# Optimization experiments

Measured on AMD Instinct MI355X. Metric: run time of the kernel, lower is better.

The kernel has to match this reference:

```python
import math
import jax
import jax.numpy as jnp
import numpy as np

B, N, NPOINT, K = 8, 2048, 512, 16
CIN = 64
MLP = [64, 128, 256]
M_W = 8    # PAConv weight-bank size
HID = 16   # scorenet hidden width
GEOM = 10  # 3 rel-xyz + 1 dist + 3 norm + 3 angles


def setup_inputs():
    key = jax.random.key(0)
    ks = jax.random.split(key, 40)
    inp = {}
    inp['xyz'] = jax.random.normal(ks[0], (B, 3, N), jnp.float32)
    inp['norm'] = jax.random.normal(ks[1], (B, 3, N), jnp.float32)
    inp['X_axis'] = jax.random.normal(ks[2], (B, 3, N), jnp.float32)
    inp['Y_axis'] = jax.random.normal(ks[3], (B, 3, N), jnp.float32)
    inp['points'] = jax.random.normal(ks[4], (B, CIN, N), jnp.float32) * 0.5
    cin = CIN
    ki = 5
    for l, cout in enumerate(MLP):
        inp['w1_%d' % l] = jax.random.normal(ks[ki], (HID, GEOM), jnp.float32) / np.sqrt(GEOM); ki += 1
        inp['b1_%d' % l] = jnp.zeros((HID,), jnp.float32)
        inp['w2_%d' % l] = jax.random.normal(ks[ki], (M_W, HID), jnp.float32) / np.sqrt(HID); ki += 1
        inp['b2_%d' % l] = jnp.zeros((M_W,), jnp.float32)
        inp['bank_%d' % l] = jax.random.normal(ks[ki], (M_W, cin, cout), jnp.float32) / np.sqrt(cin); ki += 1
        if l < len(MLP) - 1:
            inp['gamma_%d' % l] = jnp.ones((cout,), jnp.float32)
            inp['beta_%d' % l] = jnp.zeros((cout,), jnp.float32)
        cin = cout
    return inp


def _group(t, idx):
    # t: (B, C, N), idx: (B, ...) int -> (B, C, ...)
    return jax.vmap(lambda p, i: p[:, i])(t, idx)


def _fps(xyz_t, npoint):
    # xyz_t: (B, N, 3) -> (B, npoint) int32; standard iterative FPS starting at index 0
    b, n, _ = xyz_t.shape
    def body(i, c):
        idxs, dists, far = c
        idxs = idxs.at[:, i].set(far)
        centroid = jnp.take_along_axis(xyz_t, far[:, None, None], axis=1)  # (B,1,3)
        d = jnp.sum((xyz_t - centroid) ** 2, axis=-1)
        dists = jnp.minimum(dists, d)
        return idxs, dists, jnp.argmax(dists, axis=-1).astype(jnp.int32)
    idxs = jnp.zeros((b, npoint), jnp.int32)
    dists = jnp.full((b, n), 1e10, xyz_t.dtype)
    far = jnp.zeros((b,), jnp.int32)
    idxs, _, _ = jax.lax.fori_loop(0, npoint, body, (idxs, dists, far))
    return idxs


def _sqdist(a, b):
    # a: (B, P, 3), b: (B, N, 3) -> (B, P, N)
    return (jnp.sum(a ** 2, -1)[:, :, None] + jnp.sum(b ** 2, -1)[:, None, :]
            - 2.0 * jnp.einsum('bpc,bnc->bpn', a, b))


def _angles(gxyz, gn, gX, gY):
    # all (B, 3, P, K) -> (B, 3, P, K); normalized angles to z(norm)/x/y frame axes
    nn = jnp.linalg.norm(gxyz, axis=1)
    def ang(v):
        c = jnp.sum(gxyz * v, axis=1) / (nn * jnp.linalg.norm(v, axis=1) + 1e-8)
        return jnp.arccos(jnp.clip(c, -1.0, 1.0)) / math.pi
    return jnp.stack([ang(gn), ang(gX), ang(gY)], axis=1)


def _paconv(geom, feats, w1, b1, w2, b2, bank, gamma=None, beta=None, act=True):
    # ScoreNet over geometric channels -> softmax scores over M weight matrices
    h = jax.nn.relu(jnp.einsum('hg,bgpk->bhpk', w1, geom) + b1[None, :, None, None])
    s = jax.nn.softmax(jnp.einsum('mh,bhpk->bmpk', w2, h) + b2[None, :, None, None], axis=1)
    out = jnp.einsum('bcpk,mco,bmpk->bopk', feats, bank, s)
    if gamma is not None:
        mu = out.mean(axis=(0, 2, 3), keepdims=True)
        var = out.var(axis=(0, 2, 3), keepdims=True)
        out = (out - mu) / jnp.sqrt(var + 1e-5) * gamma[None, :, None, None] + beta[None, :, None, None]
    return jax.nn.relu(out) if act else out


def reference(xyz, norm, X_axis, Y_axis, points,
              w1_0, b1_0, w2_0, b2_0, bank_0, gamma_0, beta_0,
              w1_1, b1_1, w2_1, b2_1, bank_1, gamma_1, beta_1,
              w1_2, b1_2, w2_2, b2_2, bank_2):
    xyz_t = jnp.transpose(xyz, (0, 2, 1))           # (B,N,3)
    fidx = _fps(xyz_t, NPOINT)                      # (B,NPOINT)
    new_xyz = _group(xyz, fidx)                     # (B,3,NPOINT)
    sq = _sqdist(jnp.transpose(new_xyz, (0, 2, 1)), xyz_t)  # (B,NPOINT,N)
    idx = jax.lax.top_k(-sq, K)[1]                  # (B,NPOINT,K) ascending distance
    grouped_xyz = _group(xyz, idx) - new_xyz[:, :, :, None]  # (B,3,NPOINT,K)
    dist = jnp.sqrt(jnp.sum(grouped_xyz ** 2, axis=1) + 1e-10)  # (B,NPOINT,K)
    dmin = dist.min(axis=2, keepdims=True)
    dist = (dist - dmin) / (dist.max(axis=2, keepdims=True) - dmin + 1e-10)
    new_points = _group(points, idx)                # (B,CIN,NPOINT,K)
    grouped_norm = _group(norm, idx)
    grouped_X = _group(X_axis, idx)
    grouped_Y = _group(Y_axis, idx)
    grouped_angles = _angles(grouped_xyz, grouped_norm, grouped_X, grouped_Y)
    new_norm = grouped_norm[:, :, :, 0]
    new_X = grouped_X[:, :, :, 0]
    new_Y = grouped_Y[:, :, :, 0]
    geom = jnp.concatenate([grouped_xyz, dist[:, None], grouped_norm, grouped_angles], axis=1)  # (B,10,NPOINT,K)
    new_points = _paconv(geom, new_points, w1_0, b1_0, w2_0, b2_0, bank_0, gamma_0, beta_0, act=True)
    new_points = _paconv(geom, new_points, w1_1, b1_1, w2_1, b2_1, bank_1, gamma_1, beta_1, act=True)
    new_points = _paconv(geom, new_points, w1_2, b1_2, w2_2, b2_2, bank_2, None, None, act=False)
    new_points = jnp.max(new_points, axis=3)        # (B,MLP[-1],NPOINT)
    return (new_xyz, new_norm, new_X, new_Y, new_points)
```

## Files before the change

### kernel.cpp

```cpp
#include <hip/hip_runtime.h>
#include <math.h>

#define NBATCH 8
#define NPTS   2048
#define NPOINT 512
#define KNB    16
#define NROWS  (NBATCH*NPOINT*KNB)

#define TRANS_BASE  NBATCH
#define ZERO_BID    (NBATCH + 256)
#define CONV_BASE   (NBATCH + 257)
#define KNN_BASE    (NBATCH + 257 + 704)
#define MEGA_GRID   (KNN_BASE + 1024)
#define RCTR_TARGET 960

typedef unsigned short ushort_t;
typedef unsigned int   uint_t;
typedef unsigned long long ull_t;
typedef __attribute__((ext_vector_type(8))) short  short8;
typedef __attribute__((ext_vector_type(4))) float  f32x4;
typedef __attribute__((ext_vector_type(2))) float  f32x2;

#define B0_OFF 0
#define B1_OFF 32768
#define B2_OFF 98304
#define BT_TOT 360448

#define LDS_BARRIER() asm volatile("s_waitcnt lgkmcnt(0)\n\ts_barrier" ::: "memory")

__device__ __align__(16) int      g_fidx [NBATCH * NPOINT];
__device__ __align__(16) int      g_fready[NBATCH * NPOINT];
__device__            int      g_rctr = 0;
__device__ __align__(16) int      g_knn [NROWS];
__device__ __align__(16) float    g_sums[1024];
__device__ __align__(16) float    g_pT  [NBATCH * NPTS * 64];
__device__ __align__(16) float    g_S   [(size_t)3 * NROWS * 8];
__device__ __align__(16) float    g_act1[(size_t)NROWS * 64];
__device__ __align__(16) float    g_act2[(size_t)NROWS * 128];
__device__ __align__(16) ushort_t g_bankF[BT_TOT];

__device__ __forceinline__ ushort_t f2bf(float f) {
    uint_t u = __float_as_uint(f);
    return (ushort_t)((u + 0x7FFFu + ((u >> 16) & 1u)) >> 16);
}

template<int CTRL>
__device__ __forceinline__ ull_t dpp_u64(ull_t k) {
    int lo = (int)(uint_t)k;
    int hi = (int)(uint_t)(k >> 32);
    int slo = __builtin_amdgcn_update_dpp(0, lo, CTRL, 0xF, 0xF, true);
    int shi = __builtin_amdgcn_update_dpp(0, hi, CTRL, 0xF, 0xF, true);
    return ((ull_t)(uint_t)shi << 32) | (uint_t)slo;
}

__device__ __forceinline__ ull_t dpp_max_u64(ull_t key) {
    { ull_t s = dpp_u64<0x111>(key); if (s > key) key = s; }
    { ull_t s = dpp_u64<0x112>(key); if (s > key) key = s; }
    { ull_t s = dpp_u64<0x114>(key); if (s > key) key = s; }
    { ull_t s = dpp_u64<0x118>(key); if (s > key) key = s; }
    { ull_t s = dpp_u64<0x142>(key); if (s > key) key = s; }
    { ull_t s = dpp_u64<0x143>(key); if (s > key) key = s; }
    return key;
}

template<int CTRL>
__device__ __forceinline__ uint_t dpp_u32(uint_t v) {
    return (uint_t)__builtin_amdgcn_update_dpp(0, (int)v, CTRL, 0xF, 0xF, true);
}

__device__ __forceinline__ uint_t dpp_max_u32(uint_t v) {
    { uint_t s = dpp_u32<0x111>(v); if (s > v) v = s; }
    { uint_t s = dpp_u32<0x112>(v); if (s > v) v = s; }
    { uint_t s = dpp_u32<0x114>(v); if (s > v) v = s; }
    { uint_t s = dpp_u32<0x118>(v); if (s > v) v = s; }
    { uint_t s = dpp_u32<0x142>(v); if (s > v) v = s; }
    { uint_t s = dpp_u32<0x143>(v); if (s > v) v = s; }
    return v;
}

template<int COUT>
__device__ __forceinline__ void bank_frag2(const float* __restrict__ bank,
                                           uint_t* __restrict__ dst, int le) {
    const int j = le & 7;
    const int lane = (le >> 3) & 63;
    const int rem = le >> 9;
    constexpr int NTL = COUT / 16;
    const int nt = rem % NTL;
    const int kc = rem / NTL;
    const int q = lane >> 4, nlo = lane & 15;
    const int k = kc * 32 + q * 8 + j;
    const int n = nt * 16 + nlo;
    const float f0 = bank[(size_t)k * COUT + n];
    const float f1 = bank[(size_t)(k + 1) * COUT + n];
    dst[le >> 1] = (uint_t)f2bf(f0) | ((uint_t)f2bf(f1) << 16);
}

__global__ __launch_bounds__(256, 5) void mega_kernel(
    const float* __restrict__ xyz, const float* __restrict__ points,
    const float* __restrict__ bank0, const float* __restrict__ bank1,
    const float* __restrict__ bank2, float* __restrict__ dout,
    const float* __restrict__ nrm, const float* __restrict__ Xa,
    const float* __restrict__ Ya,
    const float* __restrict__ w1_0, const float* __restrict__ b1_0,
    const float* __restrict__ w2_0, const float* __restrict__ b2_0,
    const float* __restrict__ w1_1, const float* __restrict__ b1_1,
    const float* __restrict__ w2_1, const float* __restrict__ b2_1,
    const float* __restrict__ w1_2, const float* __restrict__ b1_2,
    const float* __restrict__ w2_2, const float* __restrict__ b2_2) {
    __shared__ float smem[3 * NPTS];
    __shared__ ull_t s_key[2][4];
    const int bid = blockIdx.x;
    const int t = threadIdx.x;

    if (bid >= NBATCH) {
        if (bid < ZERO_BID) {
            float (*tile)[65] = reinterpret_cast<float(*)[65]>(smem);
            const int blk = bid - TRANS_BASE;
            const int b = blk >> 5;
            const int n0 = (blk & 31) * 64;
            const int lane = t & 63, q = t >> 6;
            #pragma unroll
            for (int i = 0; i < 16; ++i) {
                int c = q * 16 + i;
                tile[c][lane] = points[(b * 64 + c) * NPTS + n0 + lane];
            }
            __syncthreads();
            #pragma unroll
            for (int i = 0; i < 16; ++i) {
                int n = q * 16 + i;
                g_pT[(size_t)(b * NPTS + n0 + n) * 64 + lane] = tile[lane][n];
            }
            __syncthreads();
            if (t == 0)
                __hip_atomic_fetch_add(&g_rctr, 1, __ATOMIC_RELEASE,
                                       __HIP_MEMORY_SCOPE_AGENT);
            return;
        } else if (bid == ZERO_BID) {
            g_sums[256 + t] = 0.0f;
            return;
        } else if (bid < KNN_BASE) {
            const int le = ((bid - CONV_BASE) * 256 + t) << 1;
            if (le < 32768) {
                bank_frag2<64>(bank0, reinterpret_cast<uint_t*>(g_bankF + B0_OFF), le);
            } else if (le < 98304) {
                bank_frag2<128>(bank1, reinterpret_cast<uint_t*>(g_bankF + B1_OFF), le - 32768);
            } else {
                bank_frag2<256>(bank2, reinterpret_cast<uint_t*>(g_bankF + B2_OFF), le - 98304);
            }
            __syncthreads();
            if (t == 0)
                __hip_atomic_fetch_add(&g_rctr, 1, __ATOMIC_RELEASE,
                                       __HIP_MEMORY_SCOPE_AGENT);
            return;
        }

        {
            const float* w1p[3] = {w1_0, w1_1, w1_2};
            const float* b1p[3] = {b1_0, b1_1, b1_2};
            const float* w2p[3] = {w2_0, w2_1, w2_2};
            const float* b2p[3] = {b2_0, b2_1, b2_2};
            #pragma unroll
            for (int l = 0; l < 3; ++l) {
                if (t < 160) smem[l * 160 + t] = w1p[l][t];
                if (t < 16)  smem[480 + l * 16 + t] = b1p[l][t];
                if (t < 128) smem[528 + l * 128 + t] = w2p[l][t];
                if (t < 8)   smem[912 + l * 8 + t] = b2p[l][t];
            }
        }
        __syncthreads();

        const int wave = (bid - KNN_BASE) * 4 + (t >> 6);
        const int lane = t & 63;
        const int b = wave >> 9;
        const int p = wave & 511;
        const float* xb = xyz + b * 3 * NPTS;

        int fv = __hip_atomic_load(&g_fready[wave], __ATOMIC_RELAXED,
                                   __HIP_MEMORY_SCOPE_AGENT);
        while (fv == 0) {
            __builtin_amdgcn_s_sleep(15);
            fv = __hip_atomic_load(&g_fready[wave], __ATOMIC_RELAXED,
                                   __HIP_MEMORY_SCOPE_AGENT);
        }
        if (lane == 0)
            __hip_atomic_store(&g_fready[wave], 0, __ATOMIC_RELAXED,
                               __HIP_MEMORY_SCOPE_AGENT);
        const int fi = (fv - 1) & (NPTS - 1);
        int nmine = 0;

        {
            #pragma clang fp contract(off)
            float ax = xb[fi];
            float ay = xb[NPTS + fi];
            float az = xb[2*NPTS + fi];
            float sa = ax*ax + ay*ay; sa = sa + az*az;
            float d[32];
            #pragma unroll
            for (int j = 0; j < 32; ++j) {
                int pp = j * 64 + lane;
                float bx = xb[pp];
                float by = xb[NPTS + pp];
                float bz = xb[2*NPTS + pp];
                float sb = bx*bx + by*by; sb = sb + bz*bz;
                float dot = ax*bx + ay*by; dot = dot + az*bz;
                float t1 = sa + sb;
                float t2 = 2.0f * dot;
                d[j] = t1 - t2;
            }
            for (int r = 0; r < KNB; ++r) {
                float best = 1e30f; int bi = 0x7fffffff;
                #pragma unroll
                for (int j = 0; j < 32; ++j) {
                    if (d[j] < best) { best = d[j]; bi = j * 64 + lane; }
                }
                uint_t ub = __float_as_uint(best);
                ub = (ub & 0x80000000u) ? ~ub : (ub | 0x80000000u);
                ull_t key = ((ull_t)(~ub) << 32) | (uint_t)(~bi);
                key = dpp_max_u64(key);
                uint_t wlo = (uint_t)__builtin_amdgcn_readlane((int)(uint_t)key, 63);
                bi = (int)(~wlo) & (NPTS - 1);
                if (lane == 0) g_knn[wave * KNB + r] = bi;
                if (lane == r) nmine = bi;
                int rl = bi & 63, rs = bi >> 6;
                if (lane == rl) {
                    #pragma unroll
                    for (int j = 0; j < 32; ++j) if (j == rs) d[j] = 1e30f;
                }
            }
        }

        {
            const int n0 = __builtin_amdgcn_readlane(nmine, 0) & (NPTS - 1);
            if (lane < 12) {
                const int arr = lane / 3, a = lane % 3;
                const float* src = (arr == 0) ? xyz : (arr == 1) ? nrm
                                 : (arr == 2) ? Xa : Ya;
                const int idx = (arr == 0) ? fi : n0;
                dout[arr * 12288 + (b*3 + a) * NPOINT + p] =
                    src[(b*3 + a) * NPTS + idx];
            }
        }

        if (lane < 16) {
            const int row = wave * KNB + lane;
            const int n = nmine & (NPTS - 1);
            const float* nb = nrm + b * 3 * NPTS;
            const float* Xb = Xa  + b * 3 * NPTS;
            const float* Yb = Ya  + b * 3 * NPTS;
            float gx, gy, gz, sq, draw, nnv;
            {
                #pragma clang fp contract(off)
                gx = xb[n]        - xb[fi];
                gy = xb[NPTS + n] - xb[NPTS + fi];
                gz = xb[2*NPTS+n] - xb[2*NPTS+fi];
                sq = gx*gx + gy*gy;
                sq = sq + gz*gz;
                draw = sqrtf(sq + 1e-10f);
                nnv = sqrtf(sq);
            }
            float dmin = draw, dmax = draw;
            #pragma unroll
            for (int m = 1; m < 16; m <<= 1) {
                dmin = fminf(dmin, __shfl_xor(dmin, m, 16));
                dmax = fmaxf(dmax, __shfl_xor(dmax, m, 16));
            }
            float dist;
            {
                #pragma clang fp contract(off)
                dist = (draw - dmin) / ((dmax - dmin) + 1e-10f);
            }
            float nx = nb[n], ny = nb[NPTS+n], nz = nb[2*NPTS+n];
            float Xx = Xb[n], Xy = Xb[NPTS+n], Xz = Xb[2*NPTS+n];
            float Yx = Yb[n], Yy = Yb[NPTS+n], Yz = Yb[2*NPTS+n];
            float g[10];
            g[0]=gx; g[1]=gy; g[2]=gz; g[3]=dist; g[4]=nx; g[5]=ny; g[6]=nz;
            {
                float vs[3][3] = {{nx,ny,nz},{Xx,Xy,Xz},{Yx,Yy,Yz}};
                #pragma unroll
                for (int a = 0; a < 3; ++a) {
                    float vx=vs[a][0], vy=vs[a][1], vz=vs[a][2];
                    float dot, nv;
                    {
                        #pragma clang fp contract(off)
                        dot = gx*vx + gy*vy; dot = dot + gz*vz;
                        float s2 = vx*vx + vy*vy; s2 = s2 + vz*vz;
                        nv = sqrtf(s2);
                    }
                    float cc = dot / (nnv * nv + 1e-8f);
                    cc = fminf(1.0f, fmaxf(-1.0f, cc));
                    g[7+a] = acosf(cc) / 3.14159274101257324f;
                }
            }
            #pragma unroll
            for (int l = 0; l < 3; ++l) {
                float h[16];
                #pragma unroll
                for (int i = 0; i < 16; ++i) {
                    float a = smem[480 + l * 16 + i];
                    #pragma unroll
                    for (int j = 0; j < 10; ++j) a += smem[l * 160 + i * 10 + j] * g[j];
                    h[i] = fmaxf(a, 0.0f);
                }
                float e[8]; float mx = -1e30f;
                #pragma unroll
                for (int m = 0; m < 8; ++m) {
                    float a = smem[912 + l * 8 + m];
                    #pragma unroll
                    for (int j = 0; j < 16; ++j) a += smem[528 + l * 128 + m * 16 + j] * h[j];
                    e[m] = a; mx = fmaxf(mx, a);
                }
                float sum = 0.0f;
                #pragma unroll
                for (int m = 0; m < 8; ++m) { e[m] = expf(e[m] - mx); sum += e[m]; }
                #pragma unroll
                for (int m = 0; m < 8; ++m)
                    g_S[(size_t)l * NROWS * 8 + (size_t)row * 8 + m] = e[m] / sum;
            }
        }

        __syncthreads();
        if (t == 0) {
            while (__hip_atomic_load(&g_rctr, __ATOMIC_ACQUIRE,
                                     __HIP_MEMORY_SCOPE_AGENT) < RCTR_TARGET)
                __builtin_amdgcn_s_sleep(8);
        }
        __syncthreads();

        {
            constexpr int NTT0 = 4;
            constexpr int CCM0 = 2;
            ushort_t (*AsP)[64][36] = reinterpret_cast<ushort_t(*)[64][36]>(smem + 1024);
            float* s_rs  = smem + 3328;
            float* s_rss = smem + 3392;
            const int w = t >> 6;
            const int q = lane >> 4, nlo = lane & 15;
            const int row0 = (bid - KNN_BASE) * 64;
            const int arow_i = t >> 2, acg = t & 3;
            const int rr = row0 + arow_i;
            const int rb = rr >> 13;
            const int rn = g_knn[rr] & (NPTS - 1);
            const size_t arow = (size_t)(rb * NPTS + rn) * 64;
            const float* Sb = g_S + (size_t)rr * 8;
            float svv[8];
            #pragma unroll
            for (int m = 0; m < 8; ++m) svv[m] = Sb[m];
            f32x4 acc[4];
            #pragma unroll
            for (int mi = 0; mi < 4; ++mi) acc[mi] = (f32x4){0.f, 0.f, 0.f, 0.f};
            const ushort_t* fbase = g_bankF + B0_OFF + lane * 8;
            union FragU { uint4 u4; uint2 u2[2]; short8 s; };
            FragU B[2];
            B[0].u4 = *reinterpret_cast<const uint4*>(fbase + (size_t)w * 512);
            float vraw[8], vnext[8];
            {
                const float* ap = g_pT + arow + acg * 8;
                float4 fa = *reinterpret_cast<const float4*>(ap);
                float4 fb = *reinterpret_cast<const float4*>(ap + 4);
                vraw[0]=fa.x; vraw[1]=fa.y; vraw[2]=fa.z; vraw[3]=fa.w;
                vraw[4]=fb.x; vraw[5]=fb.y; vraw[6]=fb.z; vraw[7]=fb.w;
            }
            int par = 0;
            for (int cc = 0; cc < CCM0; ++cc) {
                #pragma unroll
                for (int m = 0; m < 8; ++m) {
                    {
                        const float sv = svv[m];
                        uint_t* dst = reinterpret_cast<uint_t*>(&AsP[par][arow_i][acg * 8]);
                        #pragma unroll
                        for (int j = 0; j < 8; j += 2)
                            dst[j >> 1] = (uint_t)f2bf(sv * vraw[j]) |
                                          ((uint_t)f2bf(sv * vraw[j + 1]) << 16);
                    }
                    if (m == 0) {
                        const int ccn = (cc + 1 < CCM0) ? cc + 1 : cc;
                        const float* ap = g_pT + arow + ccn * 32 + acg * 8;
                        float4 fa = *reinterpret_cast<const float4*>(ap);
                        float4 fb = *reinterpret_cast<const float4*>(ap + 4);
                        vnext[0]=fa.x; vnext[1]=fa.y; vnext[2]=fa.z; vnext[3]=fa.w;
                        vnext[4]=fb.x; vnext[5]=fb.y; vnext[6]=fb.z; vnext[7]=fb.w;
                    }
                    {
                        const int kcn = (m < 7) ? ((m + 1) * CCM0 + cc)
                                                : ((cc + 1 < CCM0) ? (cc + 1) : 0);
                        B[(m + 1) & 1].u4 = *reinterpret_cast<const uint4*>(
                            fbase + (size_t)(kcn * NTT0 + w) * 512);
                    }
                    LDS_BARRIER();
                    FragU af[4];
                    #pragma unroll
                    for (int mi = 0; mi < 4; ++mi) {
                        af[mi].u2[0] = *reinterpret_cast<const uint2*>(&AsP[par][mi*16 + nlo][q*8]);
                        af[mi].u2[1] = *reinterpret_cast<const uint2*>(&AsP[par][mi*16 + nlo][q*8 + 4]);
                    }
                    #pragma unroll
                    for (int mi = 0; mi < 4; ++mi)
                        acc[mi] = __builtin_amdgcn_mfma_f32_16x16x32_bf16(
                            af[mi].s, B[m & 1].s, acc[mi], 0, 0, 0);
                    par ^= 1;
                }
                #pragma unroll
                for (int j = 0; j < 8; ++j) vraw[j] = vnext[j];
            }
            #pragma unroll
            for (int mi = 0; mi < 4; ++mi)
                #pragma unroll
                for (int r2 = 0; r2 < 4; ++r2)
                    g_act1[(size_t)(row0 + mi*16 + q*4 + r2) * 64 + w*16 + nlo] = acc[mi][r2];
            float s = 0.f, ss = 0.f;
            #pragma unroll
            for (int mi = 0; mi < 4; ++mi) {
                #pragma unroll
                for (int r2 = 0; r2 < 4; ++r2) {
                    float x = acc[mi][r2];
                    s += x; ss += x * x;
                }
            }
            s  += __shfl_xor(s, 16);  s  += __shfl_xor(s, 32);
            ss += __shfl_xor(ss, 16); ss += __shfl_xor(ss, 32);
            if (q == 0) {
                const int c = w * 16 + nlo;
                s_rs[c] = s;
                s_rss[c] = ss;
            }
            __syncthreads();
            if (t < 64) {
                atomicAdd(&g_sums[t], s_rs[t]);
                atomicAdd(&g_sums[64 + t], s_rss[t]);
            }
        }
        return;
    }

    {
        #pragma clang fp contract(off)
        const int b = bid;
        const int lane = t & 63, w = t >> 6;
        const float* xb = xyz + b * 3 * NPTS;
        float* s_x = smem;
        float* s_y = smem + NPTS;
        float* s_z = smem + 2 * NPTS;
        f32x2 xp[4], yp[4], zp[4];
        float d[8];
        {
            const float4* xq = reinterpret_cast<const float4*>(xb + t * 8);
            const float4* yq = reinterpret_cast<const float4*>(xb + NPTS + t * 8);
            const float4* zq = reinterpret_cast<const float4*>(xb + 2 * NPTS + t * 8);
            float4 a0 = xq[0], a1 = xq[1];
            float4 b0 = yq[0], b1 = yq[1];
            float4 c0 = zq[0], c1 = zq[1];
            xp[0] = (f32x2){a0.x, a0.y}; xp[1] = (f32x2){a0.z, a0.w};
            xp[2] = (f32x2){a1.x, a1.y}; xp[3] = (f32x2){a1.z, a1.w};
            yp[0] = (f32x2){b0.x, b0.y}; yp[1] = (f32x2){b0.z, b0.w};
            yp[2] = (f32x2){b1.x, b1.y}; yp[3] = (f32x2){b1.z, b1.w};
            zp[0] = (f32x2){c0.x, c0.y}; zp[1] = (f32x2){c0.z, c0.w};
            zp[2] = (f32x2){c1.x, c1.y}; zp[3] = (f32x2){c1.z, c1.w};
            *reinterpret_cast<float4*>(s_x + t * 8)     = a0;
            *reinterpret_cast<float4*>(s_x + t * 8 + 4) = a1;
            *reinterpret_cast<float4*>(s_y + t * 8)     = b0;
            *reinterpret_cast<float4*>(s_y + t * 8 + 4) = b1;
            *reinterpret_cast<float4*>(s_z + t * 8)     = c0;
            *reinterpret_cast<float4*>(s_z + t * 8 + 4) = c1;
            #pragma unroll
            for (int j = 0; j < 8; ++j) d[j] = 1e10f;
        }
        __syncthreads();
        __builtin_amdgcn_s_setprio(2);
        int far = 0;
        for (int i = 0; i < NPOINT; ++i) {
            if (t == 0) {
                g_fidx[b * NPOINT + i] = far;
                __hip_atomic_store(&g_fready[b * NPOINT + i], far + 1,
                                   __ATOMIC_RELAXED, __HIP_MEMORY_SCOPE_AGENT);
            }
            const float cx = s_x[far], cy = s_y[far], cz = s_z[far];
            const f32x2 cxp = (f32x2){cx, cx};
            const f32x2 cyp = (f32x2){cy, cy};
            const f32x2 czp = (f32x2){cz, cz};
            uint_t bb = 0u;
            #pragma unroll
            for (int a = 0; a < 4; ++a) {
                f32x2 dx = xp[a] - cxp;
                f32x2 dy = yp[a] - cyp;
                f32x2 dz = zp[a] - czp;
                f32x2 s2 = dx*dx + dy*dy;
                s2 = s2 + dz*dz;
                float dn0 = fminf(d[2*a],   s2[0]);
                float dn1 = fminf(d[2*a+1], s2[1]);
                d[2*a] = dn0; d[2*a+1] = dn1;
                uint_t u0 = __float_as_uint(dn0);
                uint_t u1 = __float_as_uint(dn1);
                bb = (u0 > bb) ? u0 : bb;
                bb = (u1 > bb) ? u1 : bb;
            }
            uint_t wm = dpp_max_u32(bb);
            const uint_t wbits = (uint_t)__builtin_amdgcn_readlane((int)wm, 63);
            int li = 8;
            #pragma unroll
            for (int j = 7; j >= 0; --j)
                li = (__float_as_uint(d[j]) == wbits) ? j : li;
            ull_t mk = __ballot(li < 8);
            const int fl = __ffsll((unsigned long long)mk) - 1;
            const int wj = __builtin_amdgcn_readlane(li, fl);
            const int wp = (((w << 6) + fl) << 3) + wj;
            if (lane == 0) s_key[i & 1][w] = ((ull_t)wbits << 32) | (uint_t)(~wp);
            LDS_BARRIER();
            const ull_t* kb = s_key[i & 1];
            ull_t k0 = kb[0], k1 = kb[1], k2 = kb[2], k3 = kb[3];
            if (k1 > k0) k0 = k1;
            if (k3 > k2) k2 = k3;
            if (k2 > k0) k0 = k2;
            far = (int)(~(uint_t)k0) & (NPTS - 1);
        }
    }
}

template<int LAYER, int CIN, int COUT>
__global__ __launch_bounds__(256) void gemm_kernel(const float* __restrict__ gamma,
                                                   const float* __restrict__ beta,
                                                   float* __restrict__ dout) {
    const float* __restrict__ A = (LAYER == 1) ? g_act1 : g_act2;
    float* __restrict__ O = (LAYER == 1) ? g_act2 : dout;
    constexpr int NTT = COUT / 16;
    constexpr int NTW = NTT / 4;
    constexpr int CCM = CIN / 32;
    constexpr int BOFF = (LAYER == 1) ? B1_OFF : B2_OFF;
    __shared__ ushort_t As[2][64][36];
    __shared__ float s_scale[CIN];
    __shared__ float s_shift[CIN];
    __shared__ float s_rs[(LAYER < 2) ? COUT : 1];
    __shared__ float s_rss[(LAYER < 2) ? COUT : 1];

    const int t = threadIdx.x;
    const int lane = t & 63, w = t >> 6;
    const int q = lane >> 4, nlo = lane & 15;
    const int row0 = blockIdx.x * 64;
    const int arow_i = t >> 2, acg = t & 3;

    if constexpr (LAYER == 2) {
        if (blockIdx.x == 0 && t < 128) g_sums[t] = 0.0f;
    }

    {
        const float* sb = (LAYER == 1) ? g_sums : (g_sums + 256);
        if (t < CIN) {
            float mu  = sb[t] * (1.0f / 65536.0f);
            float var = sb[CIN + t] * (1.0f / 65536.0f) - mu * mu;
            var = fmaxf(var, 0.0f);
            float sc = gamma[t] / sqrtf(var + 1e-5f);
            s_scale[t] = sc;
            s_shift[t] = beta[t] - mu * sc;
        }
        __syncthreads();
    }

    const size_t arow = (size_t)(row0 + arow_i) * CIN;
    const float* Sbase = g_S + (size_t)LAYER * NROWS * 8 + (size_t)(row0 + arow_i) * 8;

    float svv[8];
    #pragma unroll
    for (int m = 0; m < 8; ++m) svv[m] = Sbase[m];

    f32x4 acc[4][NTW];
    #pragma unroll
    for (int mi = 0; mi < 4; ++mi)
        #pragma unroll
        for (int ni = 0; ni < NTW; ++ni) acc[mi][ni] = (f32x4){0.f, 0.f, 0.f, 0.f};

    const ushort_t* fbase = g_bankF + BOFF + lane * 8;

    union FragU { uint4 u4; uint2 u2[2]; short8 s; };
    FragU B[2][NTW];
    #pragma unroll
    for (int ni = 0; ni < NTW; ++ni)
        B[0][ni].u4 = *reinterpret_cast<const uint4*>(fbase + (size_t)(w * NTW + ni) * 512);

    float vraw[8], vnext[8];
    {
        const float* ap = A + arow + acg * 8;
        float4 fa = *reinterpret_cast<const float4*>(ap);
        float4 fb = *reinterpret_cast<const float4*>(ap + 4);
        vraw[0]=fa.x; vraw[1]=fa.y; vraw[2]=fa.z; vraw[3]=fa.w;
        vraw[4]=fb.x; vraw[5]=fb.y; vraw[6]=fb.z; vraw[7]=fb.w;
    }

    int par = 0;
    for (int cc = 0; cc < CCM; ++cc) {
        float v[8];
        #pragma unroll
        for (int j = 0; j < 8; ++j) {
            const int c = cc * 32 + acg * 8 + j;
            v[j] = fmaxf(vraw[j] * s_scale[c] + s_shift[c], 0.f);
        }
        #pragma unroll
        for (int m = 0; m < 8; ++m) {
            {
                const float sv = svv[m];
                uint_t* dst = reinterpret_cast<uint_t*>(&As[par][arow_i][acg * 8]);
                #pragma unroll
                for (int j = 0; j < 8; j += 2)
                    dst[j >> 1] = (uint_t)f2bf(sv * v[j]) | ((uint_t)f2bf(sv * v[j+1]) << 16);
            }
            if (m == 0) {
                const int ccn = (cc + 1 < CCM) ? cc + 1 : cc;
                const float* ap = A + arow + ccn * 32 + acg * 8;
                float4 fa = *reinterpret_cast<const float4*>(ap);
                float4 fb = *reinterpret_cast<const float4*>(ap + 4);
                vnext[0]=fa.x; vnext[1]=fa.y; vnext[2]=fa.z; vnext[3]=fa.w;
                vnext[4]=fb.x; vnext[5]=fb.y; vnext[6]=fb.z; vnext[7]=fb.w;
            }
            {
                const int kcn = (m < 7) ? ((m + 1) * CCM + cc)
                                        : ((cc + 1 < CCM) ? (cc + 1) : 0);
                #pragma unroll
                for (int ni = 0; ni < NTW; ++ni)
                    B[(m + 1) & 1][ni].u4 = *reinterpret_cast<const uint4*>(
                        fbase + (size_t)(kcn * NTT + w * NTW + ni) * 512);
            }
            LDS_BARRIER();
            FragU af[4];
            #pragma unroll
            for (int mi = 0; mi < 4; ++mi) {
                af[mi].u2[0] = *reinterpret_cast<const uint2*>(&As[par][mi*16 + nlo][q*8]);
                af[mi].u2[1] = *reinterpret_cast<const uint2*>(&As[par][mi*16 + nlo][q*8 + 4]);
            }
            #pragma unroll
            for (int ni = 0; ni < NTW; ++ni)
                #pragma unroll
                for (int mi = 0; mi < 4; ++mi)
                    acc[mi][ni] = __builtin_amdgcn_mfma_f32_16x16x32_bf16(
                        af[mi].s, B[m & 1][ni].s, acc[mi][ni], 0, 0, 0);
            par ^= 1;
        }
        #pragma unroll
        for (int j = 0; j < 8; ++j) vraw[j] = vnext[j];
    }

    if constexpr (LAYER == 2) {
        const int bp0 = row0 >> 4;
        #pragma unroll
        for (int mi = 0; mi < 4; ++mi) {
            const int bp = bp0 + mi;
            const int b = bp >> 9, p = bp & 511;
            #pragma unroll
            for (int ni = 0; ni < NTW; ++ni) {
                float mv = fmaxf(fmaxf(acc[mi][ni][0], acc[mi][ni][1]),
                                 fmaxf(acc[mi][ni][2], acc[mi][ni][3]));
                mv = fmaxf(mv, __shfl_xor(mv, 16));
                mv = fmaxf(mv, __shfl_xor(mv, 32));
                if (lane < 16) {
                    const int col = w * 64 + ni * 16 + nlo;
                    O[(size_t)(b * 256 + col) * NPOINT + p] = mv;
                }
            }
        }
    } else {
        #pragma unroll
        for (int mi = 0; mi < 4; ++mi)
            #pragma unroll
            for (int ni = 0; ni < NTW; ++ni)
                #pragma unroll
                for (int r2 = 0; r2 < 4; ++r2)
                    O[(size_t)(row0 + mi*16 + q*4 + r2) * COUT + w*NTW*16 + ni*16 + nlo] = acc[mi][ni][r2];
        #pragma unroll
        for (int ni = 0; ni < NTW; ++ni) {
            float s = 0.f, ss = 0.f;
            #pragma unroll
            for (int mi = 0; mi < 4; ++mi) {
                #pragma unroll
                for (int r2 = 0; r2 < 4; ++r2) {
                    float x = acc[mi][ni][r2];
                    s += x; ss += x * x;
                }
            }
            s  += __shfl_xor(s, 16);  s  += __shfl_xor(s, 32);
            ss += __shfl_xor(ss, 16); ss += __shfl_xor(ss, 32);
            if (q == 0) {
                const int c = w * NTW * 16 + ni * 16 + nlo;
                s_rs[c] = s;
                s_rss[c] = ss;
            }
        }
        __syncthreads();
        if (t < COUT) {
            float* sb = g_sums + 256;
            atomicAdd(&sb[t], s_rs[t]);
            atomicAdd(&sb[COUT + t], s_rss[t]);
        }
    }
}

extern "C" void kernel_launch(void* const* d_in, const int* in_sizes, int n_in,
                              void* d_out, int out_size, void* d_ws, size_t ws_size,
                              hipStream_t stream) {
    const float* xyz    = (const float*)d_in[0];
    const float* nrm    = (const float*)d_in[1];
    const float* Xa     = (const float*)d_in[2];
    const float* Ya     = (const float*)d_in[3];
    const float* points = (const float*)d_in[4];
    const float* w1_0 = (const float*)d_in[5];  const float* b1_0 = (const float*)d_in[6];
    const float* w2_0 = (const float*)d_in[7];  const float* b2_0 = (const float*)d_in[8];
    const float* bank0 = (const float*)d_in[9];
    const float* g0 = (const float*)d_in[10];   const float* be0 = (const float*)d_in[11];
    const float* w1_1 = (const float*)d_in[12]; const float* b1_1 = (const float*)d_in[13];
    const float* w2_1 = (const float*)d_in[14]; const float* b2_1 = (const float*)d_in[15];
    const float* bank1 = (const float*)d_in[16];
    const float* g1 = (const float*)d_in[17];   const float* be1 = (const float*)d_in[18];
    const float* w1_2 = (const float*)d_in[19]; const float* b1_2 = (const float*)d_in[20];
    const float* w2_2 = (const float*)d_in[21]; const float* b2_2 = (const float*)d_in[22];
    const float* bank2 = (const float*)d_in[23];
    float* out = (float*)d_out;
    (void)d_ws; (void)ws_size; (void)in_sizes; (void)n_in; (void)out_size;

    mega_kernel<<<MEGA_GRID, 256, 0, stream>>>(xyz, points, bank0, bank1, bank2, out,
                                               nrm, Xa, Ya,
                                               w1_0, b1_0, w2_0, b2_0,
                                               w1_1, b1_1, w2_1, b2_1,
                                               w1_2, b1_2, w2_2, b2_2);
    gemm_kernel<1, 64, 128><<<1024, 256, 0, stream>>>(g0, be0, nullptr);
    gemm_kernel<2, 128, 256><<<1024, 256, 0, stream>>>(g1, be1, out + 49152);
}
```

Baseline: 437.8 us.

## Factor PAConv score scaling out of the GEMM A operand, applying it post-MFMA

The gemm kernel no longer rebuilds the scaled A tile in LDS for each of the 8 weight banks. It normalizes and converts the input row to bf16 once, keeps the A fragments in registers, and computes a per-bank partial product with MFMA. It then scales the output rows by the score S and accumulates in fp32. The score tensor is moved to a bank-major layout so the per-row scores can be loaded as vectors matching the MFMA output rows, and launch bounds request 2 blocks per CU. This removes repeated LDS writes and barriers, at the cost of more registers and extra fp32 FMAs per bank. It also changes rounding, since the scores are no longer applied before bf16 conversion.

```diff
diff --git a/kernel.cpp b/kernel.cpp
--- a/kernel.cpp
+++ b/kernel.cpp
@@ -34,7 +34,7 @@
 __device__ __align__(16) int      g_knn [NROWS];
 __device__ __align__(16) float    g_sums[1024];
 __device__ __align__(16) float    g_pT  [NBATCH * NPTS * 64];
-__device__ __align__(16) float    g_S   [(size_t)3 * NROWS * 8];
+__device__ __align__(16) float    g_S   [(size_t)3 * 8 * NROWS];
 __device__ __align__(16) float    g_act1[(size_t)NROWS * 64];
 __device__ __align__(16) float    g_act2[(size_t)NROWS * 128];
 __device__ __align__(16) ushort_t g_bankF[BT_TOT];
@@ -314,7 +314,7 @@
                 for (int m = 0; m < 8; ++m) { e[m] = expf(e[m] - mx); sum += e[m]; }
                 #pragma unroll
                 for (int m = 0; m < 8; ++m)
-                    g_S[(size_t)l * NROWS * 8 + (size_t)row * 8 + m] = e[m] / sum;
+                    g_S[((size_t)l * 8 + m) * NROWS + row] = e[m] / sum;
             }
         }
 
@@ -340,10 +340,9 @@
             const int rb = rr >> 13;
             const int rn = g_knn[rr] & (NPTS - 1);
             const size_t arow = (size_t)(rb * NPTS + rn) * 64;
-            const float* Sb = g_S + (size_t)rr * 8;
             float svv[8];
             #pragma unroll
-            for (int m = 0; m < 8; ++m) svv[m] = Sb[m];
+            for (int m = 0; m < 8; ++m) svv[m] = g_S[(size_t)m * NROWS + rr];
             f32x4 acc[4];
             #pragma unroll
             for (int mi = 0; mi < 4; ++mi) acc[mi] = (f32x4){0.f, 0.f, 0.f, 0.f};
@@ -515,16 +514,18 @@
 }
 
 template<int LAYER, int CIN, int COUT>
-__global__ __launch_bounds__(256) void gemm_kernel(const float* __restrict__ gamma,
-                                                   const float* __restrict__ beta,
-                                                   float* __restrict__ dout) {
+__global__ __launch_bounds__(256, 2) void gemm_kernel(const float* __restrict__ gamma,
+                                                      const float* __restrict__ beta,
+                                                      float* __restrict__ dout) {
     const float* __restrict__ A = (LAYER == 1) ? g_act1 : g_act2;
     float* __restrict__ O = (LAYER == 1) ? g_act2 : dout;
     constexpr int NTT = COUT / 16;
     constexpr int NTW = NTT / 4;
     constexpr int CCM = CIN / 32;
+    constexpr int PADC = CIN + 4;
+    constexpr int CPT = CIN / 4;
     constexpr int BOFF = (LAYER == 1) ? B1_OFF : B2_OFF;
-    __shared__ ushort_t As[2][64][36];
+    __shared__ ushort_t As[64][PADC];
     __shared__ float s_scale[CIN];
     __shared__ float s_shift[CIN];
     __shared__ float s_rs[(LAYER < 2) ? COUT : 1];
@@ -553,12 +554,36 @@
         __syncthreads();
     }
 
-    const size_t arow = (size_t)(row0 + arow_i) * CIN;
-    const float* Sbase = g_S + (size_t)LAYER * NROWS * 8 + (size_t)(row0 + arow_i) * 8;
-
-    float svv[8];
+    {
+        const size_t arow = (size_t)(row0 + arow_i) * CIN;
+        const float* ap = A + arow + acg * CPT;
+        uint_t* dst = reinterpret_cast<uint_t*>(&As[arow_i][acg * CPT]);
+        #pragma unroll
+        for (int jj = 0; jj < CPT; jj += 8) {
+            float4 fa = *reinterpret_cast<const float4*>(ap + jj);
+            float4 fb = *reinterpret_cast<const float4*>(ap + jj + 4);
+            float v[8] = {fa.x, fa.y, fa.z, fa.w, fb.x, fb.y, fb.z, fb.w};
+            #pragma unroll
+            for (int k2 = 0; k2 < 8; ++k2) {
+                const int c = acg * CPT + jj + k2;
+                v[k2] = fmaxf(v[k2] * s_scale[c] + s_shift[c], 0.f);
+            }
+            #pragma unroll
+            for (int k2 = 0; k2 < 8; k2 += 2)
+                dst[(jj + k2) >> 1] = (uint_t)f2bf(v[k2]) | ((uint_t)f2bf(v[k2+1]) << 16);
+        }
+    }
+    LDS_BARRIER();
+
+    union FragU { uint4 u4; uint2 u2[2]; short8 s; };
+    FragU af[CCM][4];
     #pragma unroll
-    for (int m = 0; m < 8; ++m) svv[m] = Sbase[m];
+    for (int kc = 0; kc < CCM; ++kc)
+        #pragma unroll
+        for (int mi = 0; mi < 4; ++mi) {
+            af[kc][mi].u2[0] = *reinterpret_cast<const uint2*>(&As[mi*16 + nlo][kc*32 + q*8]);
+            af[kc][mi].u2[1] = *reinterpret_cast<const uint2*>(&As[mi*16 + nlo][kc*32 + q*8 + 4]);
+        }
 
     f32x4 acc[4][NTW];
     #pragma unroll
@@ -567,72 +592,44 @@
         for (int ni = 0; ni < NTW; ++ni) acc[mi][ni] = (f32x4){0.f, 0.f, 0.f, 0.f};
 
     const ushort_t* fbase = g_bankF + BOFF + lane * 8;
-
-    union FragU { uint4 u4; uint2 u2[2]; short8 s; };
-    FragU B[2][NTW];
+    const float* Sbase = g_S + (size_t)LAYER * 8 * NROWS;
+
+    FragU Bf[2][CCM];
     #pragma unroll
-    for (int ni = 0; ni < NTW; ++ni)
-        B[0][ni].u4 = *reinterpret_cast<const uint4*>(fbase + (size_t)(w * NTW + ni) * 512);
-
-    float vraw[8], vnext[8];
-    {
-        const float* ap = A + arow + acg * 8;
-        float4 fa = *reinterpret_cast<const float4*>(ap);
-        float4 fb = *reinterpret_cast<const float4*>(ap + 4);
-        vraw[0]=fa.x; vraw[1]=fa.y; vraw[2]=fa.z; vraw[3]=fa.w;
-        vraw[4]=fb.x; vraw[5]=fb.y; vraw[6]=fb.z; vraw[7]=fb.w;
-    }
-
-    int par = 0;
-    for (int cc = 0; cc < CCM; ++cc) {
-        float v[8];
+    for (int cc = 0; cc < CCM; ++cc)
+        Bf[0][cc].u4 = *reinterpret_cast<const uint4*>(
+            fbase + (size_t)(cc * NTT + w * NTW) * 512);
+
+    #pragma unroll
+    for (int m = 0; m < 8; ++m) {
+        f32x4 Sv[4];
         #pragma unroll
-        for (int j = 0; j < 8; ++j) {
-            const int c = cc * 32 + acg * 8 + j;
-            v[j] = fmaxf(vraw[j] * s_scale[c] + s_shift[c], 0.f);
-        }
+        for (int mi = 0; mi < 4; ++mi)
+            Sv[mi] = *reinterpret_cast<const f32x4*>(
+                Sbase + (size_t)m * NROWS + row0 + mi*16 + q*4);
         #pragma unroll
-        for (int m = 0; m < 8; ++m) {
-            {
-                const float sv = svv[m];
-                uint_t* dst = reinterpret_cast<uint_t*>(&As[par][arow_i][acg * 8]);
-                #pragma unroll
-                for (int j = 0; j < 8; j += 2)
-                    dst[j >> 1] = (uint_t)f2bf(sv * v[j]) | ((uint_t)f2bf(sv * v[j+1]) << 16);
-            }
-            if (m == 0) {
-                const int ccn = (cc + 1 < CCM) ? cc + 1 : cc;
-                const float* ap = A + arow + ccn * 32 + acg * 8;
-                float4 fa = *reinterpret_cast<const float4*>(ap);
-                float4 fb = *reinterpret_cast<const float4*>(ap + 4);
-                vnext[0]=fa.x; vnext[1]=fa.y; vnext[2]=fa.z; vnext[3]=fa.w;
-                vnext[4]=fb.x; vnext[5]=fb.y; vnext[6]=fb.z; vnext[7]=fb.w;
-            }
-            {
-                const int kcn = (m < 7) ? ((m + 1) * CCM + cc)
-                                        : ((cc + 1 < CCM) ? (cc + 1) : 0);
-                #pragma unroll
-                for (int ni = 0; ni < NTW; ++ni)
-                    B[(m + 1) & 1][ni].u4 = *reinterpret_cast<const uint4*>(
-                        fbase + (size_t)(kcn * NTT + w * NTW + ni) * 512);
-            }
-            LDS_BARRIER();
-            FragU af[4];
-            #pragma unroll
-            for (int mi = 0; mi < 4; ++mi) {
-                af[mi].u2[0] = *reinterpret_cast<const uint2*>(&As[par][mi*16 + nlo][q*8]);
-                af[mi].u2[1] = *reinterpret_cast<const uint2*>(&As[par][mi*16 + nlo][q*8 + 4]);
-            }
-            #pragma unroll
-            for (int ni = 0; ni < NTW; ++ni)
+        for (int ni = 0; ni < NTW; ++ni) {
+            const int s = m * NTW + ni;
+            if (s + 1 < 8 * NTW) {
+                const int ns = s + 1, nm = ns / NTW, nni = ns % NTW;
+                #pragma unroll
+                for (int cc = 0; cc < CCM; ++cc)
+                    Bf[(s + 1) & 1][cc].u4 = *reinterpret_cast<const uint4*>(
+                        fbase + (size_t)((nm * CCM + cc) * NTT + w * NTW + nni) * 512);
+            }
+            f32x4 a2[4];
+            #pragma unroll
+            for (int mi = 0; mi < 4; ++mi) a2[mi] = (f32x4){0.f, 0.f, 0.f, 0.f};
+            #pragma unroll
+            for (int cc = 0; cc < CCM; ++cc)
                 #pragma unroll
                 for (int mi = 0; mi < 4; ++mi)
-                    acc[mi][ni] = __builtin_amdgcn_mfma_f32_16x16x32_bf16(
-                        af[mi].s, B[m & 1][ni].s, acc[mi][ni], 0, 0, 0);
-            par ^= 1;
-        }
-        #pragma unroll
-        for (int j = 0; j < 8; ++j) vraw[j] = vnext[j];
+                    a2[mi] = __builtin_amdgcn_mfma_f32_16x16x32_bf16(
+                        af[cc][mi].s, Bf[s & 1][cc].s, a2[mi], 0, 0, 0);
+            #pragma unroll
+            for (int mi = 0; mi < 4; ++mi)
+                acc[mi][ni] += Sv[mi] * a2[mi];
+        }
     }
 
     if constexpr (LAYER == 2) {
```

New measurement: 974.8 us. 123% more time.
